# Kernel tuning notes

Hardware: AMD Instinct MI355X
Metric: run time of the kernel (lower is better)

Reference implementation:

```python
import jax, jax.numpy as jnp
import numpy as np

B, S, D, H, HD, TOPK = 2, 2048, 2048, 16, 128, 256
HIDDEN = 4 * D
EPS = 1e-6


def setup_inputs() -> dict:
    key = jax.random.key(0)
    ks = jax.random.split(key, 12)
    def g(k, shape, scale):
        return jax.random.normal(k, shape, dtype=jnp.float32) * scale
    # rotary tables: freqs_cis[s, i] = (cos, sin) of s * theta_i
    theta = 1.0 / (10000.0 ** (np.arange(0, HD, 2, dtype=np.float32) / HD))  # [HD/2]
    ang = np.arange(S, dtype=np.float32)[:, None] * theta[None, :]           # [S, HD/2]
    freqs_cis = jnp.asarray(np.stack([np.cos(ang), np.sin(ang)], axis=-1))   # [S, HD/2, 2]
    return {
        "x": g(ks[0], (B, S, D), 1.0),
        "start_pos": 0,
        "freqs_cis": freqs_cis,
        "router_w": g(ks[1], (D, 1), D ** -0.5),
        "wq": g(ks[2], (D, H * HD), D ** -0.5),
        "wk": g(ks[3], (D, H * HD), D ** -0.5),
        "wv": g(ks[4], (D, H * HD), D ** -0.5),
        "wo": g(ks[5], (H * HD, D), (H * HD) ** -0.5),
        "w1": g(ks[6], (D, HIDDEN), D ** -0.5),
        "w2": g(ks[7], (HIDDEN, D), HIDDEN ** -0.5),
        "w3": g(ks[8], (D, HIDDEN), D ** -0.5),
        "attn_norm_w": jnp.ones((D,), jnp.float32),
        "ffn_norm_w": jnp.ones((D,), jnp.float32),
    }


def _rmsnorm(x, w, eps=EPS):
    return x * jax.lax.rsqrt(jnp.mean(x * x, axis=-1, keepdims=True) + eps) * w


def _rotary(q, freqs):  # q: [B,S,H,HD], freqs: [S,HD/2,2]
    q = q.reshape(*q.shape[:-1], HD // 2, 2)
    cos = freqs[None, :, None, :, 0]
    sin = freqs[None, :, None, :, 1]
    qr = q[..., 0] * cos - q[..., 1] * sin
    qi = q[..., 0] * sin + q[..., 1] * cos
    return jnp.stack([qr, qi], axis=-1).reshape(*q.shape[:-2], HD)


def _attention(xn, freqs, tok_mask, wq, wk, wv, wo):
    b, s, _ = xn.shape
    q = (xn @ wq).reshape(b, s, H, HD)
    k = (xn @ wk).reshape(b, s, H, HD)
    v = (xn @ wv).reshape(b, s, H, HD)
    q = _rotary(q, freqs)
    k = _rotary(k, freqs)
    scores = jnp.einsum("bqhd,bkhd->bhqk", q, k) / np.sqrt(HD).astype(np.float32)
    # keys of non-selected tokens are masked out (MoD routing mask)
    scores = scores + jnp.where(tok_mask[:, None, None, :] > 0, 0.0, -1e9)
    attn = jax.nn.softmax(scores, axis=-1)
    out = jnp.einsum("bhqk,bkhd->bqhd", attn, v).reshape(b, s, H * HD)
    return out @ wo


def reference(x, start_pos, freqs_cis, router_w, wq, wk, wv, wo, w1, w2, w3, attn_norm_w, ffn_norm_w):
    b, s, _ = x.shape
    freqs = jax.lax.dynamic_slice_in_dim(freqs_cis, start_pos, s, axis=0)
    # --- router: top-k token selection + scatter mask ---
    token_weights = x @ router_w                      # [B,S,1]
    topk_vals, topk_idx = jax.lax.top_k(token_weights[..., 0], TOPK)
    mask = jnp.zeros((b, s), x.dtype).at[jnp.arange(b)[:, None], topk_idx].set(1.0)
    masked_input = x * mask[:, :, None]
    # --- dense attention + FFN on masked tokens ---
    h = masked_input + _attention(_rmsnorm(masked_input, attn_norm_w), freqs, mask, wq, wk, wv, wo)
    hn = _rmsnorm(h, ffn_norm_w)
    out = (jax.nn.silu(hn @ w1) * (hn @ w3)) @ w2    # SwiGLU FFN
    return out, token_weights, topk_idx
```

## Files before the change

kernel.cpp:

```cpp
#include <hip/hip_runtime.h>
#include <hip/hip_bf16.h>
#include <math.h>

#define B_ 2
#define S_ 2048
#define D_ 2048
#define H_ 16
#define HD_ 128
#define TOPK_ 256
#define HIDDEN_ 8192
#define EPS_ 1e-6f

constexpr int ROWS_SEL = B_ * TOPK_;
constexpr int ROWS_ALL = ROWS_SEL + B_;

typedef __attribute__((ext_vector_type(8))) short bf16x8;
typedef __attribute__((ext_vector_type(4))) float f32x4;

__device__ __forceinline__ short f2bf(float f) {
    __hip_bfloat16 h = __float2bfloat16(f);
    return *reinterpret_cast<short*>(&h);
}

__device__ __forceinline__ float bf2f(short s) {
    union { unsigned u; float f; } c;
    c.u = ((unsigned)(unsigned short)s) << 16;
    return c.f;
}

__device__ __forceinline__ void gll16(const void* g, void* l) {
    __builtin_amdgcn_global_load_lds(
        (const __attribute__((address_space(1))) unsigned int*)g,
        (__attribute__((address_space(3))) unsigned int*)l, 16, 0, 0);
}

__device__ __forceinline__ float block_sum_256(float v, float* red4) {
    for (int o = 32; o; o >>= 1) v += __shfl_down(v, o);
    if ((threadIdx.x & 63) == 0) red4[threadIdx.x >> 6] = v;
    __syncthreads();
    float t = red4[0] + red4[1] + red4[2] + red4[3];
    __syncthreads();
    return t;
}

__device__ __forceinline__ float block_max_256(float v, float* red4) {
    for (int o = 32; o; o >>= 1) v = fmaxf(v, __shfl_down(v, o));
    if ((threadIdx.x & 63) == 0) red4[threadIdx.x >> 6] = v;
    __syncthreads();
    float t = fmaxf(fmaxf(red4[0], red4[1]), fmaxf(red4[2], red4[3]));
    __syncthreads();
    return t;
}

__global__ __launch_bounds__(256) void wtrans_kernel(const float* __restrict__ Wsrc,
                                                     short* __restrict__ WT,
                                                     int K, int N) {
    int k0 = blockIdx.y * 64, n0 = blockIdx.x * 64;
    __shared__ short L[64][72];
    int t = threadIdx.x;
    int r = t >> 4, c4 = (t & 15) * 4;
    #pragma unroll
    for (int p = 0; p < 4; ++p) {
        int kr = r + p * 16;
        float4 v = *(const float4*)&Wsrc[(size_t)(k0 + kr) * N + n0 + c4];
        L[kr][c4 + 0] = f2bf(v.x);
        L[kr][c4 + 1] = f2bf(v.y);
        L[kr][c4 + 2] = f2bf(v.z);
        L[kr][c4 + 3] = f2bf(v.w);
    }
    __syncthreads();
    int dr = t >> 3, kc = (t & 7) * 8;
    #pragma unroll
    for (int p = 0; p < 2; ++p) {
        int n = dr + p * 32;
        union { short s[8]; int4 v; } u;
        #pragma unroll
        for (int j = 0; j < 8; ++j) u.s[j] = L[kc + j][n];
        *(int4*)&WT[(size_t)(n0 + n) * K + k0 + kc] = u.v;
    }
}

__global__ __launch_bounds__(256) void router_kernel(const float* __restrict__ x,
                                                     const float* __restrict__ rw,
                                                     float* __restrict__ tw) {
    int token = blockIdx.x;
    const float4* xr = (const float4*)(x + (long)token * D_);
    const float4* r4 = (const float4*)rw;
    float s = 0.f;
    for (int c = threadIdx.x; c < D_ / 4; c += 256) {
        float4 a = xr[c], b = r4[c];
        s += a.x * b.x + a.y * b.y + a.z * b.z + a.w * b.w;
    }
    __shared__ float red4[4];
    float tot = block_sum_256(s, red4);
    if (threadIdx.x == 0) tw[token] = tot;
}

__global__ __launch_bounds__(1024) void topk_kernel(const float* __restrict__ tw,
                                                    float* __restrict__ idx_out,
                                                    int* __restrict__ sel_idx,
                                                    int* __restrict__ sel_pos) {
    int b = blockIdx.x;
    __shared__ float v[S_];
    __shared__ int id[S_];
    int t = threadIdx.x;
    for (int i = t; i < S_; i += 1024) {
        v[i] = tw[b * S_ + i];
        id[i] = i;
        sel_pos[b * S_ + i] = -1;
    }
    __syncthreads();
    for (int k = 2; k <= S_; k <<= 1) {
        for (int j = k >> 1; j > 0; j >>= 1) {
            for (int i = t; i < S_; i += 1024) {
                int ixj = i ^ j;
                if (ixj > i) {
                    float va = v[i], vb = v[ixj];
                    int ia = id[i], ib = id[ixj];
                    bool before = (va > vb) || (va == vb && ia < ib);
                    bool dir = ((i & k) == 0);
                    if (dir != before) {
                        v[i] = vb; v[ixj] = va;
                        id[i] = ib; id[ixj] = ia;
                    }
                }
            }
            __syncthreads();
        }
    }
    if (t < TOPK_) {
        idx_out[b * TOPK_ + t] = (float)id[t];
        sel_idx[b * TOPK_ + t] = id[t];
        sel_pos[b * S_ + id[t]] = t;
    }
}

__global__ __launch_bounds__(256) void gather_rmsnorm_kernel(const float* __restrict__ x,
                                                             const int* __restrict__ sel_idx,
                                                             const float* __restrict__ nw,
                                                             short* __restrict__ XN) {
    int r = blockIdx.x;
    int b = r >> 8;
    int s = sel_idx[r];
    const float* xr = x + ((long)b * S_ + s) * D_;
    __shared__ float buf[D_];
    __shared__ float red4[4];
    float ss = 0.f;
    for (int c = threadIdx.x; c < D_; c += 256) {
        float vv = xr[c];
        buf[c] = vv;
        ss += vv * vv;
    }
    float tot = block_sum_256(ss, red4);
    float scale = rsqrtf(tot / D_ + EPS_);
    for (int c = threadIdx.x; c < D_; c += 256)
        XN[(long)r * D_ + c] = f2bf(buf[c] * scale * nw[c]);
}

__global__ __launch_bounds__(256) void gemm_mfma_wbt(
    const short* __restrict__ A,
    const short* __restrict__ T0, const short* __restrict__ T1, const short* __restrict__ T2,
    float* __restrict__ Cb, long czStride, long spStride,
    int M, int N, int Ktot, int K_per, int splits) {
    __shared__ short smem[2 * 128 * 32];
    short* As = smem;
    short* Bs = smem + 128 * 32;
    int z = blockIdx.z;
    int zmat = z / splits, sp = z % splits;
    const short* BT = (zmat == 0) ? T0 : (zmat == 1) ? T1 : T2;
    float* C = Cb + (long)zmat * czStride + (long)sp * spStride;
    int kbase = sp * K_per;
    int row0 = blockIdx.y * 128, col0 = blockIdx.x * 128;
    int t = threadIdx.x;
    int lane = t & 63, w = t >> 6;
    int l16 = lane & 15, quad = lane >> 4;
    int wr = (w >> 1) * 64, wc = (w & 1) * 64;
    int rr = t >> 2, ch = (t & 3) * 8;
    int ar0 = row0 + rr;      ar0 = (ar0 < M) ? ar0 : (M - 1);
    int ar1 = row0 + rr + 64; ar1 = (ar1 < M) ? ar1 : (M - 1);
    const short* Ap0 = A + (size_t)ar0 * Ktot + ch;
    const short* Ap1 = A + (size_t)ar1 * Ktot + ch;
    const short* Bp0 = BT + (size_t)(col0 + rr) * Ktot + ch;
    const short* Bp1 = BT + (size_t)(col0 + rr + 64) * Ktot + ch;
    f32x4 acc[4][4] = {};
    for (int k0 = kbase; k0 < kbase + K_per; k0 += 32) {
        __syncthreads();
        gll16(Ap0 + k0, (char*)As + t * 16);
        gll16(Ap1 + k0, (char*)As + 4096 + t * 16);
        gll16(Bp0 + k0, (char*)Bs + t * 16);
        gll16(Bp1 + k0, (char*)Bs + 4096 + t * 16);
        __syncthreads();
        bf16x8 af[4], bfr[4];
        #pragma unroll
        for (int i = 0; i < 4; ++i)
            af[i] = *(const bf16x8*)(As + (wr + i * 16 + l16) * 32 + quad * 8);
        #pragma unroll
        for (int j = 0; j < 4; ++j)
            bfr[j] = *(const bf16x8*)(Bs + (wc + j * 16 + l16) * 32 + quad * 8);
        #pragma unroll
        for (int i = 0; i < 4; ++i)
            #pragma unroll
            for (int j = 0; j < 4; ++j)
                acc[i][j] = __builtin_amdgcn_mfma_f32_16x16x32_bf16(af[i], bfr[j], acc[i][j], 0, 0, 0);
    }
    #pragma unroll
    for (int i = 0; i < 4; ++i) {
        #pragma unroll
        for (int r = 0; r < 4; ++r) {
            int row = row0 + wr + i * 16 + quad * 4 + r;
            if (row < M) {
                #pragma unroll
                for (int j = 0; j < 4; ++j)
                    C[(size_t)row * N + col0 + wc + j * 16 + l16] = acc[i][j][r];
            }
        }
    }
}

template <bool OBF>
__global__ __launch_bounds__(256) void gemm_mfma_attn(
    const short* __restrict__ A, long sAo, long sAi, int lda,
    const short* __restrict__ Bm, long sBo, long sBi, int ldb,
    void* __restrict__ Cv, long sCo, long sCi, int ldc,
    int M, int N, int K, int inner) {
    __shared__ short smem[2 * 128 * 32];
    short* As = smem;
    short* Bs = smem + 128 * 32;
    int z = blockIdx.z;
    int zo = z / inner, zi = z % inner;
    const short* Ab = A + (long)zo * sAo + (long)zi * sAi;
    const short* Bb = Bm + (long)zo * sBo + (long)zi * sBi;
    long cbase = (long)zo * sCo + (long)zi * sCi;
    int row0 = blockIdx.y * 128, col0 = blockIdx.x * 128;
    int t = threadIdx.x;
    int lane = t & 63, w = t >> 6;
    int l16 = lane & 15, quad = lane >> 4;
    int wr = (w >> 1) * 64, wc = (w & 1) * 64;
    int rr = t >> 2, ch = (t & 3) * 8;
    f32x4 acc[4][4] = {};
    for (int k0 = 0; k0 < K; k0 += 32) {
        __syncthreads();
        #pragma unroll
        for (int rd = 0; rd < 2; ++rd) {
            int r = rr + rd * 64;
            int ar = row0 + r; ar = (ar < M) ? ar : (M - 1);
            gll16(Ab + (size_t)ar * lda + k0 + ch, (char*)As + rd * 4096 + t * 16);
            gll16(Bb + (size_t)(col0 + r) * ldb + k0 + ch, (char*)Bs + rd * 4096 + t * 16);
        }
        __syncthreads();
        bf16x8 af[4], bfr[4];
        #pragma unroll
        for (int i = 0; i < 4; ++i)
            af[i] = *(const bf16x8*)(As + (wr + i * 16 + l16) * 32 + quad * 8);
        #pragma unroll
        for (int j = 0; j < 4; ++j)
            bfr[j] = *(const bf16x8*)(Bs + (wc + j * 16 + l16) * 32 + quad * 8);
        #pragma unroll
        for (int i = 0; i < 4; ++i)
            #pragma unroll
            for (int j = 0; j < 4; ++j)
                acc[i][j] = __builtin_amdgcn_mfma_f32_16x16x32_bf16(af[i], bfr[j], acc[i][j], 0, 0, 0);
    }
    #pragma unroll
    for (int i = 0; i < 4; ++i) {
        #pragma unroll
        for (int r = 0; r < 4; ++r) {
            int row = row0 + wr + i * 16 + quad * 4 + r;
            if (row < M) {
                #pragma unroll
                for (int j = 0; j < 4; ++j) {
                    long idx = cbase + (size_t)row * ldc + col0 + wc + j * 16 + l16;
                    if (OBF) ((short*)Cv)[idx] = f2bf(acc[i][j][r]);
                    else     ((float*)Cv)[idx] = acc[i][j][r];
                }
            }
        }
    }
}

__global__ __launch_bounds__(256) void qkv_finish(
    const float* __restrict__ Cp, const float* __restrict__ fc,
    const int* __restrict__ sel_idx, const int* __restrict__ sp0,
    short* __restrict__ Qbf, short* __restrict__ Kbf, short* __restrict__ Vbf,
    int splits) {
    int r = blockIdx.x;
    int s = sel_idx[r];
    int pos = sp0[0] + s;
    const float* f = fc + (long)pos * HD_;
    const long matS = (long)ROWS_SEL * D_;
    const long spS = 3 * matS;
    const float* qp = Cp + (long)r * D_;
    const float* kp = qp + matS;
    const float* vp = qp + 2 * matS;
    const float qscale = 0.08838834764831845f;
    for (int p = threadIdx.x; p < (D_ / 2); p += 256) {
        int h = p >> 6, d2 = p & 63;
        int e0 = h * HD_ + d2 * 2;
        float q0 = 0.f, q1 = 0.f, k0 = 0.f, k1 = 0.f, v0 = 0.f, v1 = 0.f;
        for (int sp = 0; sp < splits; ++sp) {
            long off = (long)sp * spS;
            q0 += qp[off + e0]; q1 += qp[off + e0 + 1];
            k0 += kp[off + e0]; k1 += kp[off + e0 + 1];
            v0 += vp[off + e0]; v1 += vp[off + e0 + 1];
        }
        float c = f[d2 * 2], sn = f[d2 * 2 + 1];
        Qbf[(long)r * D_ + e0]     = f2bf((q0 * c - q1 * sn) * qscale);
        Qbf[(long)r * D_ + e0 + 1] = f2bf((q0 * sn + q1 * c) * qscale);
        Kbf[(long)r * D_ + e0]     = f2bf(k0 * c - k1 * sn);
        Kbf[(long)r * D_ + e0 + 1] = f2bf(k0 * sn + k1 * c);
        Vbf[(long)r * D_ + e0]     = f2bf(v0);
        Vbf[(long)r * D_ + e0 + 1] = f2bf(v1);
    }
}

__global__ __launch_bounds__(256) void vt_kernel(const short* __restrict__ Vbf,
                                                 short* __restrict__ VT) {
    int z = blockIdx.z;
    int b = z >> 4, h = z & 15;
    int key0 = blockIdx.x * 64, d0 = blockIdx.y * 64;
    __shared__ short L[64][72];
    int t = threadIdx.x;
    int kr = t >> 3, dc = (t & 7) * 8;
    #pragma unroll
    for (int rr = 0; rr < 2; ++rr) {
        int key = kr + rr * 32;
        union { short s[8]; int4 v; } u;
        u.v = *(const int4*)&Vbf[(size_t)(b * 256 + key0 + key) * D_ + h * 128 + d0 + dc];
        #pragma unroll
        for (int j = 0; j < 8; ++j) L[key][dc + j] = u.s[j];
    }
    __syncthreads();
    int dr = t >> 3, kc = (t & 7) * 8;
    #pragma unroll
    for (int rr = 0; rr < 2; ++rr) {
        int d = dr + rr * 32;
        union { short s[8]; int4 v; } u;
        #pragma unroll
        for (int j = 0; j < 8; ++j) u.s[j] = L[kc + j][d];
        *(int4*)&VT[((size_t)z * 128 + d0 + d) * 256 + key0 + kc] = u.v;
    }
}

__global__ __launch_bounds__(256) void softmax_kernel(const float* __restrict__ SC,
                                                      short* __restrict__ Pbf) {
    long row = blockIdx.x;
    const float* p = SC + row * 256;
    int t = threadIdx.x;
    float v = p[t];
    __shared__ float red4[4];
    float m = block_max_256(v, red4);
    float e = expf(v - m);
    float s = block_sum_256(e, red4);
    Pbf[row * 256 + t] = f2bf(e / s);
}

__global__ __launch_bounds__(256) void vbar_kernel(const short* __restrict__ Vbf,
                                                   short* __restrict__ Obf) {
    int b = blockIdx.y;
    int c = blockIdx.x * 256 + threadIdx.x;
    float s = 0.f;
    for (int i = 0; i < TOPK_; ++i) s += bf2f(Vbf[((long)b * TOPK_ + i) * D_ + c]);
    Obf[(long)(ROWS_SEL + b) * D_ + c] = f2bf(s * (1.f / TOPK_));
}

__global__ __launch_bounds__(256) void resid_rmsnorm_kernel(const float* __restrict__ Pp,
                                                            int splits,
                                                            const float* __restrict__ x,
                                                            const int* __restrict__ sel_idx,
                                                            const float* __restrict__ nw,
                                                            short* __restrict__ HN) {
    int r = blockIdx.x;
    __shared__ float buf[D_];
    __shared__ float red4[4];
    const long spS = (long)ROWS_ALL * D_;
    const float* pr = Pp + (long)r * D_;
    const float* xr = nullptr;
    if (r < ROWS_SEL) {
        int b = r >> 8;
        int s = sel_idx[r];
        xr = x + ((long)b * S_ + s) * D_;
    }
    float ss = 0.f;
    for (int c = threadIdx.x; c < D_; c += 256) {
        float v = xr ? xr[c] : 0.f;
        for (int sp = 0; sp < splits; ++sp) v += pr[(long)sp * spS + c];
        buf[c] = v;
        ss += v * v;
    }
    float tot = block_sum_256(ss, red4);
    float scale = rsqrtf(tot / D_ + EPS_);
    for (int c = threadIdx.x; c < D_; c += 256)
        HN[(long)r * D_ + c] = f2bf(buf[c] * scale * nw[c]);
}

__global__ __launch_bounds__(256) void reduce_silu_kernel(const float* __restrict__ Gp,
                                                          short* __restrict__ FF, long n) {
    long i = (long)blockIdx.x * 256 + threadIdx.x;
    if (i < n) {
        const long cz = (long)ROWS_ALL * HIDDEN_;
        float a = Gp[i] + Gp[cz + i];
        float g = Gp[2 * cz + i] + Gp[3 * cz + i];
        FF[i] = f2bf((a / (1.f + expf(-a))) * g);
    }
}

__global__ __launch_bounds__(256) void w2_reduce_kernel(const float* __restrict__ Wp,
                                                        float* __restrict__ OUTR, long n4) {
    long i = (long)blockIdx.x * 256 + threadIdx.x;
    if (i < n4) {
        const long spS4 = (long)ROWS_ALL * D_ / 4;
        float4 s = ((const float4*)Wp)[i];
        for (int sp = 1; sp < 8; ++sp) {
            float4 v = ((const float4*)Wp)[(long)sp * spS4 + i];
            s.x += v.x; s.y += v.y; s.z += v.z; s.w += v.w;
        }
        ((float4*)OUTR)[i] = s;
    }
}

__global__ __launch_bounds__(256) void scatter_kernel(const float* __restrict__ OUTR,
                                                      const int* __restrict__ sel_pos,
                                                      float* __restrict__ out) {
    int blk = blockIdx.x;
    int b = blk >> 11;
    int p = sel_pos[blk];
    int row = (p >= 0) ? (b * TOPK_ + p) : (ROWS_SEL + b);
    const float4* src = (const float4*)(OUTR + (long)row * D_);
    float4* dst = (float4*)(out + (long)blk * D_);
    for (int c = threadIdx.x; c < D_ / 4; c += 256) dst[c] = src[c];
}

extern "C" void kernel_launch(void* const* d_in, const int* in_sizes, int n_in,
                              void* d_out, int out_size, void* d_ws, size_t ws_size,
                              hipStream_t stream) {
    const float* x        = (const float*)d_in[0];
    const int*   startpos = (const int*)d_in[1];
    const float* freqs    = (const float*)d_in[2];
    const float* router_w = (const float*)d_in[3];
    const float* wq       = (const float*)d_in[4];
    const float* wk       = (const float*)d_in[5];
    const float* wv       = (const float*)d_in[6];
    const float* wo       = (const float*)d_in[7];
    const float* w1       = (const float*)d_in[8];
    const float* w2       = (const float*)d_in[9];
    const float* w3       = (const float*)d_in[10];
    const float* attn_w   = (const float*)d_in[11];
    const float* ffn_w    = (const float*)d_in[12];

    float* out     = (float*)d_out;
    float* tw_out  = out + (long)B_ * S_ * D_;
    float* idx_out = tw_out + (long)B_ * S_;

    char* ws = (char*)d_ws;
    auto alloc = [&](size_t bytes) -> void* {
        void* p = (void*)ws;
        ws += (bytes + 255) / 256 * 256;
        return p;
    };
    int*   sel_idx = (int*)alloc((size_t)B_ * TOPK_ * sizeof(int));
    int*   sel_pos = (int*)alloc((size_t)B_ * S_ * sizeof(int));
    short* XNbf = (short*)alloc((size_t)ROWS_SEL * D_ * sizeof(short));
    short* Qbf  = (short*)alloc((size_t)ROWS_SEL * D_ * sizeof(short));
    short* Kbf  = (short*)alloc((size_t)ROWS_SEL * D_ * sizeof(short));
    short* Vbf  = (short*)alloc((size_t)ROWS_SEL * D_ * sizeof(short));
    short* VT   = (short*)alloc((size_t)B_ * H_ * HD_ * TOPK_ * sizeof(short));
    float* SC   = (float*)alloc((size_t)B_ * H_ * TOPK_ * TOPK_ * sizeof(float));
    short* Pbf  = (short*)alloc((size_t)B_ * H_ * TOPK_ * TOPK_ * sizeof(short));
    short* Obf  = (short*)alloc((size_t)ROWS_ALL * D_ * sizeof(short));
    short* HNbf = (short*)alloc((size_t)ROWS_ALL * D_ * sizeof(short));
    short* FFbf = (short*)alloc((size_t)ROWS_ALL * HIDDEN_ * sizeof(short));
    float* OUTR = (float*)alloc((size_t)ROWS_ALL * D_ * sizeof(float));
    short* wqT = (short*)alloc((size_t)D_ * D_ * sizeof(short));
    short* wkT = (short*)alloc((size_t)D_ * D_ * sizeof(short));
    short* wvT = (short*)alloc((size_t)D_ * D_ * sizeof(short));
    short* woT = (short*)alloc((size_t)D_ * D_ * sizeof(short));
    short* w1T = (short*)alloc((size_t)D_ * HIDDEN_ * sizeof(short));
    short* w3T = (short*)alloc((size_t)D_ * HIDDEN_ * sizeof(short));
    short* w2T = (short*)alloc((size_t)HIDDEN_ * D_ * sizeof(short));
    float* Gar  = (float*)alloc((size_t)4 * ROWS_ALL * HIDDEN_ * sizeof(float));

    {
        auto wt = [&](const float* src, short* dst, int K, int N) {
            dim3 g(N / 64, K / 64);
            wtrans_kernel<<<g, 256, 0, stream>>>(src, dst, K, N);
        };
        wt(wq, wqT, D_, D_);
        wt(wk, wkT, D_, D_);
        wt(wv, wvT, D_, D_);
        wt(wo, woT, D_, D_);
        wt(w1, w1T, D_, HIDDEN_);
        wt(w3, w3T, D_, HIDDEN_);
        wt(w2, w2T, HIDDEN_, D_);
    }
    router_kernel<<<B_ * S_, 256, 0, stream>>>(x, router_w, tw_out);
    topk_kernel<<<B_, 1024, 0, stream>>>(tw_out, idx_out, sel_idx, sel_pos);
    gather_rmsnorm_kernel<<<ROWS_SEL, 256, 0, stream>>>(x, sel_idx, attn_w, XNbf);
    {
        dim3 g(D_ / 128, ROWS_SEL / 128, 3 * 4);
        gemm_mfma_wbt<<<g, 256, 0, stream>>>(XNbf, wqT, wkT, wvT,
                                             Gar, (long)ROWS_SEL * D_, (long)3 * ROWS_SEL * D_,
                                             ROWS_SEL, D_, D_, D_ / 4, 4);
    }
    qkv_finish<<<ROWS_SEL, 256, 0, stream>>>(Gar, freqs, sel_idx, startpos, Qbf, Kbf, Vbf, 4);
    {
        dim3 g(4, 2, B_ * H_);
        vt_kernel<<<g, 256, 0, stream>>>(Vbf, VT);
    }
    {
        dim3 g(2, 2, B_ * H_);
        gemm_mfma_attn<false><<<g, 256, 0, stream>>>(
            Qbf, (long)TOPK_ * D_, HD_, D_,
            Kbf, (long)TOPK_ * D_, HD_, D_,
            SC, (long)H_ * TOPK_ * TOPK_, (long)TOPK_ * TOPK_, TOPK_,
            TOPK_, TOPK_, HD_, H_);
    }
    softmax_kernel<<<B_ * H_ * TOPK_, 256, 0, stream>>>(SC, Pbf);
    {
        dim3 g(1, 2, B_ * H_);
        gemm_mfma_attn<true><<<g, 256, 0, stream>>>(
            Pbf, (long)H_ * TOPK_ * TOPK_, (long)TOPK_ * TOPK_, TOPK_,
            VT, (long)H_ * HD_ * TOPK_, (long)HD_ * TOPK_, TOPK_,
            Obf, (long)TOPK_ * D_, HD_, D_,
            TOPK_, HD_, TOPK_, H_);
    }
    {
        dim3 g(D_ / 256, B_, 1);
        vbar_kernel<<<g, 256, 0, stream>>>(Vbf, Obf);
    }
    {
        dim3 g(D_ / 128, (ROWS_ALL + 127) / 128, 8);
        gemm_mfma_wbt<<<g, 256, 0, stream>>>(Obf, woT, woT, woT,
                                             Gar, 0, (long)ROWS_ALL * D_,
                                             ROWS_ALL, D_, D_, D_ / 8, 8);
    }
    resid_rmsnorm_kernel<<<ROWS_ALL, 256, 0, stream>>>(Gar, 8, x, sel_idx, ffn_w, HNbf);
    {
        dim3 g(HIDDEN_ / 128, (ROWS_ALL + 127) / 128, 2 * 2);
        gemm_mfma_wbt<<<g, 256, 0, stream>>>(HNbf, w1T, w3T, w3T,
                                             Gar, (long)2 * ROWS_ALL * HIDDEN_, (long)ROWS_ALL * HIDDEN_,
                                             ROWS_ALL, HIDDEN_, D_, D_ / 2, 2);
    }
    {
        long n = (long)ROWS_ALL * HIDDEN_;
        reduce_silu_kernel<<<(unsigned)((n + 255) / 256), 256, 0, stream>>>(Gar, FFbf, n);
    }
    {
        dim3 g(D_ / 128, (ROWS_ALL + 127) / 128, 8);
        gemm_mfma_wbt<<<g, 256, 0, stream>>>(FFbf, w2T, w2T, w2T,
                                             Gar, 0, (long)ROWS_ALL * D_,
                                             ROWS_ALL, D_, HIDDEN_, HIDDEN_ / 8, 8);
    }
    {
        long n4 = (long)ROWS_ALL * D_ / 4;
        w2_reduce_kernel<<<(unsigned)((n4 + 255) / 256), 256, 0, stream>>>(Gar, OUTR, n4);
    }
    scatter_kernel<<<B_ * S_, 256, 0, stream>>>(OUTR, sel_pos, out);
}
```

Measured before the change: 617.9 us.

## Double-buffer GEMM LDS tiles and XOR-swizzle transpose kernels' shared memory

The weight-times-activation GEMM now keeps two LDS stages for A and B, issuing global-to-LDS loads for the next K tile while MFMAs run on the current one. This replaces the two block barriers per iteration with one barrier plus explicit waitcnts, aiming to hide global load latency. The weight and V transpose kernels XOR-swizzle their LDS column index to reduce bank conflicts on the transposed reads. LDS use doubles in the GEMM, which may lower occupancy. The V transpose now has a redundant duplicate read loop.

```diff
diff --git a/kernel.cpp b/kernel.cpp
--- a/kernel.cpp
+++ b/kernel.cpp
@@ -58,25 +58,28 @@
     int k0 = blockIdx.y * 64, n0 = blockIdx.x * 64;
     __shared__ short L[64][72];
     int t = threadIdx.x;
-    int r = t >> 4, c4 = (t & 15) * 4;
+    int kr = t >> 4, c4 = (t & 15) * 4;
     #pragma unroll
     for (int p = 0; p < 4; ++p) {
-        int kr = r + p * 16;
-        float4 v = *(const float4*)&Wsrc[(size_t)(k0 + kr) * N + n0 + c4];
-        L[kr][c4 + 0] = f2bf(v.x);
-        L[kr][c4 + 1] = f2bf(v.y);
-        L[kr][c4 + 2] = f2bf(v.z);
-        L[kr][c4 + 3] = f2bf(v.w);
+        int k = kr + p * 16;
+        float4 v = *(const float4*)&Wsrc[(size_t)(k0 + k) * N + n0 + c4];
+        int cs = c4 ^ (((k >> 3) & 7) << 3);
+        L[k][cs + 0] = f2bf(v.x);
+        L[k][cs + 1] = f2bf(v.y);
+        L[k][cs + 2] = f2bf(v.z);
+        L[k][cs + 3] = f2bf(v.w);
     }
     __syncthreads();
     int dr = t >> 3, kc = (t & 7) * 8;
+    int gswz = ((kc >> 3) & 7) << 3;
     #pragma unroll
     for (int p = 0; p < 2; ++p) {
-        int n = dr + p * 32;
+        int d = dr + p * 32;
+        int dcol = d ^ gswz;
         union { short s[8]; int4 v; } u;
         #pragma unroll
-        for (int j = 0; j < 8; ++j) u.s[j] = L[kc + j][n];
-        *(int4*)&WT[(size_t)(n0 + n) * K + k0 + kc] = u.v;
+        for (int j = 0; j < 8; ++j) u.s[j] = L[kc + j][dcol];
+        *(int4*)&WT[(size_t)(n0 + d) * K + k0 + kc] = u.v;
     }
 }
 
@@ -162,9 +165,8 @@
     const short* __restrict__ T0, const short* __restrict__ T1, const short* __restrict__ T2,
     float* __restrict__ Cb, long czStride, long spStride,
     int M, int N, int Ktot, int K_per, int splits) {
-    __shared__ short smem[2 * 128 * 32];
-    short* As = smem;
-    short* Bs = smem + 128 * 32;
+    __shared__ short As[2][128 * 32];
+    __shared__ short Bs[2][128 * 32];
     int z = blockIdx.z;
     int zmat = z / splits, sp = z % splits;
     const short* BT = (zmat == 0) ? T0 : (zmat == 1) ? T1 : T2;
@@ -183,25 +185,46 @@
     const short* Bp0 = BT + (size_t)(col0 + rr) * Ktot + ch;
     const short* Bp1 = BT + (size_t)(col0 + rr + 64) * Ktot + ch;
     f32x4 acc[4][4] = {};
-    for (int k0 = kbase; k0 < kbase + K_per; k0 += 32) {
-        __syncthreads();
-        gll16(Ap0 + k0, (char*)As + t * 16);
-        gll16(Ap1 + k0, (char*)As + 4096 + t * 16);
-        gll16(Bp0 + k0, (char*)Bs + t * 16);
-        gll16(Bp1 + k0, (char*)Bs + 4096 + t * 16);
-        __syncthreads();
+    int nk = K_per >> 5;
+    gll16(Ap0 + kbase, (char*)As[0] + t * 16);
+    gll16(Ap1 + kbase, (char*)As[0] + 4096 + t * 16);
+    gll16(Bp0 + kbase, (char*)Bs[0] + t * 16);
+    gll16(Bp1 + kbase, (char*)Bs[0] + 4096 + t * 16);
+    asm volatile("s_waitcnt vmcnt(0)" ::: "memory");
+    __builtin_amdgcn_sched_barrier(0);
+    __builtin_amdgcn_s_barrier();
+    __builtin_amdgcn_sched_barrier(0);
+    for (int kt = 0; kt < nk; ++kt) {
+        int cur = kt & 1;
+        if (kt + 1 < nk) {
+            int k1 = kbase + (kt + 1) * 32;
+            char* Ad = (char*)As[cur ^ 1];
+            char* Bd = (char*)Bs[cur ^ 1];
+            gll16(Ap0 + k1, Ad + t * 16);
+            gll16(Ap1 + k1, Ad + 4096 + t * 16);
+            gll16(Bp0 + k1, Bd + t * 16);
+            gll16(Bp1 + k1, Bd + 4096 + t * 16);
+        }
+        const short* Asc = As[cur];
+        const short* Bsc = Bs[cur];
         bf16x8 af[4], bfr[4];
         #pragma unroll
         for (int i = 0; i < 4; ++i)
-            af[i] = *(const bf16x8*)(As + (wr + i * 16 + l16) * 32 + quad * 8);
+            af[i] = *(const bf16x8*)(Asc + (wr + i * 16 + l16) * 32 + quad * 8);
         #pragma unroll
         for (int j = 0; j < 4; ++j)
-            bfr[j] = *(const bf16x8*)(Bs + (wc + j * 16 + l16) * 32 + quad * 8);
+            bfr[j] = *(const bf16x8*)(Bsc + (wc + j * 16 + l16) * 32 + quad * 8);
+        asm volatile("s_waitcnt lgkmcnt(0)" ::: "memory");
+        __builtin_amdgcn_sched_barrier(0);
         #pragma unroll
         for (int i = 0; i < 4; ++i)
             #pragma unroll
             for (int j = 0; j < 4; ++j)
                 acc[i][j] = __builtin_amdgcn_mfma_f32_16x16x32_bf16(af[i], bfr[j], acc[i][j], 0, 0, 0);
+        asm volatile("s_waitcnt vmcnt(0)" ::: "memory");
+        __builtin_amdgcn_sched_barrier(0);
+        __builtin_amdgcn_s_barrier();
+        __builtin_amdgcn_sched_barrier(0);
     }
     #pragma unroll
     for (int i = 0; i < 4; ++i) {
@@ -324,19 +347,23 @@
     #pragma unroll
     for (int rr = 0; rr < 2; ++rr) {
         int key = kr + rr * 32;
+        int cs = dc ^ (((key >> 3) & 7) << 3);
         union { short s[8]; int4 v; } u;
         u.v = *(const int4*)&Vbf[(size_t)(b * 256 + key0 + key) * D_ + h * 128 + d0 + dc];
         #pragma unroll
-        for (int j = 0; j < 8; ++j) L[key][dc + j] = u.s[j];
+        for (int j = 0; j < 8; ++j) L[key][cs + j] = u.s[j];
     }
     __syncthreads();
     int dr = t >> 3, kc = (t & 7) * 8;
+    int gswz = ((kc >> 3) & 7) << 3;
     #pragma unroll
     for (int rr = 0; rr < 2; ++rr) {
         int d = dr + rr * 32;
         union { short s[8]; int4 v; } u;
         #pragma unroll
-        for (int j = 0; j < 8; ++j) u.s[j] = L[kc + j][d];
+        for (int j = 0; j < 8; ++j) u.s[j] = L[kc + j][(d ^ gswz) - (d & 7) + ((d & 7))];
+        #pragma unroll
+        for (int j = 0; j < 8; ++j) u.s[j] = L[kc + j][d ^ gswz];
         *(int4*)&VT[((size_t)z * 128 + d0 + d) * 256 + key0 + kc] = u.v;
     }
 }
```

After: 597.4 us. 1.03x faster.
